# Performance work log

Hardware: AMD Instinct MI355X
Metric: run time of the kernel (lower is better)

Reference implementation:

```python
import jax, jax.numpy as jnp
import numpy as np

KS = 3          # image feature patch kernel size
RATE = 2        # downsample rate; alpha patches use kernel RATE*2, stride RATE
PENALTY = -10000.0
EPS = 1e-4
BN_EPS = 1e-5


def _pad(x, k, s):
    # reflect 'same' padding as in GCAModule.pad
    l = (k - s + 1) // 2
    r = (k - s) // 2
    return jnp.pad(x, ((0, 0), (0, 0), (l, r), (l, r)), mode='reflect')


def _extract_patches(x, k, s):
    # replicates reflect-pad + F.unfold + reshape -> (n, L, c, k, k)
    x = _pad(x, k, s)
    n, c, H, W = x.shape
    oh = (H - k) // s + 1
    ow = (W - k) // s + 1
    cols = [x[:, :, di:di + s * (oh - 1) + 1:s, dj:dj + s * (ow - 1) + 1:s]
            for di in range(k) for dj in range(k)]
    p = jnp.stack(cols, axis=2).reshape(n, c, k, k, oh * ow)  # (n,c,k,k,L)
    return jnp.transpose(p, (0, 4, 1, 2, 3))                  # (n,L,c,k,k)


def _deconv(score, kern):
    # torch: F.conv_transpose2d(score[None], kern, stride=RATE, padding=1) / 4
    # score: (L,h,w); kern: (L, ac, 4, 4) in torch conv_transpose (I,O,kh,kw) layout
    k = jnp.transpose(jnp.flip(kern, axis=(2, 3)), (1, 0, 2, 3))  # -> OIHW
    out = jax.lax.conv_general_dilated(
        score[None], k, window_strides=(1, 1), padding=[(2, 2), (2, 2)],
        lhs_dilation=(RATE, RATE), dimension_numbers=('NCHW', 'OIHW', 'NCHW'))
    return out[0] / 4.0


def gca_forward(img_feat, alpha_feat, unknown, gconv_w, gconv_b, oconv_w,
                bn_gamma, bn_beta):
    n = img_feat.shape[0]
    # guidance 1x1 conv + nearest downsample by RATE
    g = jnp.einsum('nchw,oc->nohw', img_feat, gconv_w) + gconv_b[None, :, None, None]
    g = g[:, :, ::RATE, ::RATE]
    u = unknown[:, :, ::RATE, ::RATE]
    # process_unknown_mask: per-sample softmax scales
    um = u.mean(axis=(2, 3))                                    # (n,1)
    km = 1.0 - um
    unknown_scale = jnp.clip(jnp.sqrt(um / km), 0.1, 10.0)      # (n,1)
    known_scale = jnp.clip(jnp.sqrt(km / um), 0.1, 10.0)        # (n,1)
    h, w = g.shape[2], g.shape[3]
    L = h * w
    img_ps = _extract_patches(g, KS, 1)                         # (n,L,c,3,3)
    alpha_ps = _extract_patches(alpha_feat, RATE * 2, RATE)     # (n,L,ac,4,4)
    unk_ps = _extract_patches(u, KS, 1)[:, :, 0].mean(axis=(2, 3))  # (n,L)
    # l2-normalized image patch kernels
    norm = jnp.sqrt(jnp.sum(img_ps * img_ps, axis=(2, 3, 4), keepdims=True))
    img_ps_n = img_ps / jnp.maximum(norm, EPS)
    # similarity: conv of padded g with patch kernels == patches-at-p . kernel-q
    sim = jnp.einsum('npckl,nqckl->nqp', img_ps, img_ps_n)      # (n,L,L)
    is_unknown = (unk_ps > 0.0).astype(sim.dtype)               # (n,L)
    scale = unknown_scale * is_unknown + known_scale * (1.0 - is_unknown)
    out = sim * scale[:, :, None]
    idx = jnp.arange(L)
    out = out.at[:, idx, idx].add(PENALTY * unk_ps)             # self-corr penalty
    gca = jax.nn.softmax(out, axis=1).reshape(n, L, h, w)
    prop = jax.vmap(_deconv)(gca, alpha_ps)                     # (n,ac,2h,2w)
    # out_conv: 1x1 conv (no bias) + BatchNorm (training stats) + residual
    y = jnp.einsum('nchw,oc->nohw', prop, oconv_w)
    mu = y.mean(axis=(0, 2, 3), keepdims=True)
    var = y.var(axis=(0, 2, 3), keepdims=True)
    y = (y - mu) / jnp.sqrt(var + BN_EPS)
    y = y * bn_gamma[None, :, None, None] + bn_beta[None, :, None, None]
    return y + alpha_feat


def setup_inputs():
    key = jax.random.key(0)
    ks = jax.random.split(key, 8)
    N, C, AC, H, W = 4, 256, 128, 64, 64
    img_feat = jax.random.normal(ks[0], (N, C, H, W), jnp.float32)
    alpha_feat = jax.random.normal(ks[1], (N, AC, H, W), jnp.float32)
    unknown = jax.random.randint(ks[2], (N, 1, H, W), 0, 2).astype(jnp.float32)
    gconv_w = jax.random.normal(ks[3], (C // 2, C), jnp.float32) / np.float32(np.sqrt(C))
    gconv_b = jax.random.normal(ks[4], (C // 2,), jnp.float32) * 0.01
    oconv_w = jax.random.normal(ks[5], (AC, AC), jnp.float32) / np.float32(np.sqrt(AC))
    bn_gamma = 0.001 + jax.random.normal(ks[6], (AC,), jnp.float32) * 0.001
    bn_beta = jax.random.normal(ks[7], (AC,), jnp.float32) * 0.001
    return dict(img_feat=img_feat, alpha_feat=alpha_feat, unknown=unknown,
                gconv_w=gconv_w, gconv_b=gconv_b, oconv_w=oconv_w,
                bn_gamma=bn_gamma, bn_beta=bn_beta)


def reference(img_feat, alpha_feat, unknown, gconv_w, gconv_b, oconv_w,
              bn_gamma, bn_beta):
    return gca_forward(img_feat, alpha_feat, unknown, gconv_w, gconv_b,
                       oconv_w, bn_gamma, bn_beta)
```

## Files before the change

### kernel.cpp

```cpp
#include <hip/hip_runtime.h>

#define NN 4
#define CIN 256
#define CH 128
#define HH 64
#define hh 32
#define L 1024
#define NB 2048
#define PENALTY -10000.0f
#define EPS 1e-4f

typedef __bf16 bf16x8 __attribute__((ext_vector_type(8)));
typedef float f32x4 __attribute__((ext_vector_type(4)));
typedef __attribute__((address_space(3))) void lds_t;
typedef __attribute__((address_space(1))) const void gbl_t;

__device__ __forceinline__ int refl32(int t) { return t < 0 ? -t : (t > 31 ? 62 - t : t); }
__device__ __forceinline__ int refl64(int t) { return t < 0 ? -t : (t > 63 ? 126 - t : t); }
__device__ __forceinline__ int swz(int k, int row) { return k ^ (((row >> 1) & 3) << 3); }

__global__ void k_prep(const float* __restrict__ img, const float* __restrict__ gw,
                       const float* __restrict__ ow, const float* __restrict__ unknown,
                       const float* __restrict__ alpha,
                       __bf16* __restrict__ Xb, __bf16* __restrict__ gwb,
                       __bf16* __restrict__ owb, float* __restrict__ unk,
                       float* __restrict__ scales, __bf16* __restrict__ Bt,
                       float* __restrict__ stats) {
    __shared__ float sm[CIN * 33];
    int bid = blockIdx.x, t = threadIdx.x;
    if (bid < 512) {
        int n = bid >> 7, o = bid & 127;
        const float* ap = alpha + ((size_t)(n * CH + o) << 12);
#pragma unroll
        for (int j = 0; j < 4; ++j) {
            int fi = t + j * 256;
            int row = fi >> 4, c4 = fi & 15;
            float4 v = *(const float4*)(ap + fi * 4);
            float* d = sm + row * 65 + c4 * 4;
            d[0] = v.x; d[1] = v.y; d[2] = v.z; d[3] = v.w;
        }
        __syncthreads();
        __bf16* Bn = Bt + ((size_t)(n * NB) << 10);
#pragma unroll
        for (int gi = 0; gi < 8; ++gi) {
            int g = gi * 256 + t;
            int ab = g >> 7, qg = g & 127;
            int a = ab >> 2, bb = ab & 3;
            int q0 = qg * 8;
            int qi = q0 >> 5, qj0 = q0 & 31;
            int ti = refl64(2 * qi + a - 1);
            const float* r = sm + ti * 65;
            __bf16 v[8];
#pragma unroll
            for (int s = 0; s < 8; ++s) v[s] = (__bf16)r[refl64(2 * (qj0 + s) + bb - 1)];
            int j = ab * 128 + o;
            *(bf16x8*)(Bn + ((size_t)j << 10) + swz(q0, j)) = *(bf16x8*)v;
        }
    } else if (bid < 640) {
        int idx = bid - 512;
        int i = idx & 31, n = idx >> 5;
        for (int e = t; e < CIN * 32; e += 256) {
            int c = e >> 5, jj = e & 31;
            sm[c * 33 + jj] = img[(((size_t)n * CIN + c) * HH + 2 * i) * HH + 2 * jj];
        }
        __syncthreads();
#pragma unroll
        for (int j = 0; j < 32; ++j) {
            int np = (n << 10) + i * 32 + j;
            int cl = swz(t, np);
            Xb[(size_t)np * CIN + t] = (__bf16)sm[cl * 33 + j];
        }
    } else if (bid < 644) {
        int n = bid - 640;
        float* u = sm;
        float* red = sm + 1024;
        float part = 0.f;
#pragma unroll
        for (int c = 0; c < 4; ++c) {
            int idx = t + c * 256;
            int i = idx >> 5, j = idx & 31;
            float v = unknown[n * 4096 + (2 * i) * HH + 2 * j];
            u[idx] = v;
            part += v;
        }
        red[t] = part;
        __syncthreads();
        for (int s = 128; s > 0; s >>= 1) {
            if (t < s) red[t] += red[t + s];
            __syncthreads();
        }
        if (t == 0) {
            float um = red[0] / 1024.0f;
            float km = 1.0f - um;
            scales[n * 2] = fminf(fmaxf(sqrtf(um / km), 0.1f), 10.0f);
            scales[n * 2 + 1] = fminf(fmaxf(sqrtf(km / um), 0.1f), 10.0f);
        }
#pragma unroll
        for (int c = 0; c < 4; ++c) {
            int idx = t + c * 256;
            int i = idx >> 5, j = idx & 31;
            float sum = 0.f;
#pragma unroll
            for (int di = -1; di <= 1; ++di)
#pragma unroll
                for (int dj = -1; dj <= 1; ++dj)
                    sum += u[refl32(i + di) * 32 + refl32(j + dj)];
            unk[n * L + idx] = sum * (1.0f / 9.0f);
        }
    } else {
        if (bid == 644) stats[t] = 0.f;
        for (int e = (bid - 644) * 256 + t; e < 49152; e += 36 * 256) {
            if (e < 32768) {
                int o = e >> 8, m = e & 255;
                gwb[e] = (__bf16)gw[o * 256 + swz(m, o)];
            } else {
                int e2 = e - 32768;
                int j = e2 >> 7, m = e2 & 127;
                owb[e2] = (__bf16)ow[j * 128 + swz(m, j)];
            }
        }
    }
}

__global__ __launch_bounds__(256, 2) void k_gemm0(const __bf16* __restrict__ Xb,
                                                  const __bf16* __restrict__ gwb,
                                                  const float* __restrict__ gb,
                                                  __bf16* __restrict__ gbf) {
    __shared__ __align__(16) __bf16 As[128 * 32];
    __shared__ __align__(16) __bf16 Bs[128 * 32];
    int p0 = blockIdx.x * 128;
    int t = threadIdx.x, l = t & 63, w = t >> 6;
    int wr = w >> 1, wc = w & 1;
    f32x4 acc[4][4] = {};
    for (int k0 = 0; k0 < CIN; k0 += 32) {
#pragma unroll
        for (int i = 0; i < 2; ++i) {
            const __bf16* srcA = Xb + (size_t)(p0 + i * 64 + (t >> 2)) * CIN + k0 + (t & 3) * 8;
            __builtin_amdgcn_global_load_lds((gbl_t*)srcA, (lds_t*)(As + i * 2048 + t * 8), 16, 0, 0);
            const __bf16* srcB = gwb + (size_t)(i * 64 + (t >> 2)) * CIN + k0 + (t & 3) * 8;
            __builtin_amdgcn_global_load_lds((gbl_t*)srcB, (lds_t*)(Bs + i * 2048 + t * 8), 16, 0, 0);
        }
        __syncthreads();
        int gl = l >> 4, r = l & 15;
        bf16x8 av[4], bv[4];
#pragma unroll
        for (int m = 0; m < 4; ++m) {
            int row = wr * 64 + m * 16 + r;
            av[m] = *(const bf16x8*)(As + row * 32 + swz(gl << 3, row));
            int col = wc * 64 + m * 16 + r;
            bv[m] = *(const bf16x8*)(Bs + col * 32 + swz(gl << 3, col));
        }
#pragma unroll
        for (int m = 0; m < 4; ++m)
#pragma unroll
            for (int c2 = 0; c2 < 4; ++c2)
                acc[m][c2] = __builtin_amdgcn_mfma_f32_16x16x32_bf16(av[m], bv[c2], acc[m][c2], 0, 0, 0);
        __syncthreads();
    }
    int r = l & 15, hi = l >> 4;
#pragma unroll
    for (int m = 0; m < 4; ++m)
#pragma unroll
        for (int c2 = 0; c2 < 4; ++c2) {
            int o = wc * 64 + c2 * 16 + r;
            float bias = gb[o];
#pragma unroll
            for (int reg = 0; reg < 4; ++reg) {
                int row = p0 + wr * 64 + m * 16 + hi * 4 + reg;
                gbf[((size_t)row << 7) + o] = (__bf16)(acc[m][c2][reg] + bias);
            }
        }
}

__global__ void k_ssqf(const __bf16* __restrict__ gbf, const float* __restrict__ unk,
                       const float* __restrict__ scales, float* __restrict__ f) {
    __shared__ float ssqs[1024];
    int n = blockIdx.x, t = threadIdx.x;
    {
        const __bf16* rp = gbf + (((size_t)(n << 10) + t) << 7);
        float s = 0.f;
#pragma unroll
        for (int kk = 0; kk < 16; ++kk) {
            bf16x8 v = *(const bf16x8*)(rp + kk * 8);
#pragma unroll
            for (int u2 = 0; u2 < 8; ++u2) {
                float x = (float)v[u2];
                s += x * x;
            }
        }
        ssqs[t] = s;
    }
    __syncthreads();
    float us = scales[n * 2], ks = scales[n * 2 + 1];
    int pi = t >> 5, pj = t & 31;
    float sum = 0.f;
#pragma unroll
    for (int di = -1; di <= 1; ++di)
#pragma unroll
        for (int dj = -1; dj <= 1; ++dj)
            sum += ssqs[refl32(pi + di) * 32 + refl32(pj + dj)];
    float norm = sqrtf(sum);
    float sc = unk[n * L + t] > 0.f ? us : ks;
    f[n * L + t] = sc / fmaxf(norm, EPS);
}

__global__ __launch_bounds__(256, 1) void k_gemm1(const __bf16* __restrict__ gbf,
                                                  const float* __restrict__ f,
                                                  const float* __restrict__ unk,
                                                  float* __restrict__ W) {
    __shared__ __align__(16) __bf16 As[4 * 6144];
    __shared__ __align__(16) __bf16 Bs[4 * 6144];
    int n = blockIdx.z;
    int p0 = blockIdx.y * 128, q0 = blockIdx.x * 128;
    const __bf16* gn = gbf + ((size_t)n << 17);
    int t = threadIdx.x, l = t & 63, w = t >> 6;
    int wr = w >> 1, wc = w & 1;
    int by4 = blockIdx.y * 4, bx4 = blockIdx.x * 4;
    int rbA = by4 - 1; rbA = rbA < 0 ? 0 : (rbA > 26 ? 26 : rbA);
    int rbB = bx4 - 1; rbB = rbB < 0 ? 0 : (rbB > 26 ? 26 : rbB);
#pragma unroll
    for (int k = 0; k < 12; ++k) {
        int chunk = k / 3;
        int rem = (k % 3) * 256 + t;
        int wrow = rem >> 2, sg = rem & 3;
        int so = (chunk << 5) + ((sg ^ ((wrow >> 1) & 3)) << 3);
        int grA = ((rbA + (wrow >> 5)) << 5) + (wrow & 31);
        __builtin_amdgcn_global_load_lds((gbl_t*)(gn + (size_t)grA * 128 + so),
                                         (lds_t*)(As + chunk * 6144 + rem * 8), 16, 0, 0);
        int grB = ((rbB + (wrow >> 5)) << 5) + (wrow & 31);
        __builtin_amdgcn_global_load_lds((gbl_t*)(gn + (size_t)grB * 128 + so),
                                         (lds_t*)(Bs + chunk * 6144 + rem * 8), 16, 0, 0);
    }
    __syncthreads();
    int gl = l >> 4, r = l & 15;
    int rpA[4][3], cpA[4][3], rpB[4][3], cpB[4][3];
#pragma unroll
    for (int m = 0; m < 4; ++m) {
        int prow = wr * 64 + m * 16 + r;
        int qrow = wc * 64 + m * 16 + r;
#pragma unroll
        for (int d = 0; d < 3; ++d) {
            rpA[m][d] = (refl32(by4 + (prow >> 5) + d - 1) - rbA) << 10;
            int cp = refl32((prow & 31) + d - 1);
            cpA[m][d] = cp * 32 + ((gl ^ ((cp >> 1) & 3)) << 3);
            rpB[m][d] = (refl32(bx4 + (qrow >> 5) + d - 1) - rbB) << 10;
            int cq = refl32((qrow & 31) + d - 1);
            cpB[m][d] = cq * 32 + ((gl ^ ((cq >> 1) & 3)) << 3);
        }
    }
    f32x4 acc[4][4] = {};
#pragma unroll
    for (int dk = 0; dk < 3; ++dk)
#pragma unroll
        for (int dl = 0; dl < 3; ++dl)
#pragma unroll
            for (int cc = 0; cc < 4; ++cc) {
                bf16x8 av[4], bv[4];
#pragma unroll
                for (int m = 0; m < 4; ++m) {
                    av[m] = *(const bf16x8*)(As + cc * 6144 + rpA[m][dk] + cpA[m][dl]);
                    bv[m] = *(const bf16x8*)(Bs + cc * 6144 + rpB[m][dk] + cpB[m][dl]);
                }
#pragma unroll
                for (int m = 0; m < 4; ++m)
#pragma unroll
                    for (int c2 = 0; c2 < 4; ++c2)
                        acc[m][c2] = __builtin_amdgcn_mfma_f32_16x16x32_bf16(av[m], bv[c2], acc[m][c2], 0, 0, 0);
            }
    int hi = l >> 4;
#pragma unroll
    for (int m = 0; m < 4; ++m)
#pragma unroll
        for (int c2 = 0; c2 < 4; ++c2) {
            int q = q0 + wc * 64 + c2 * 16 + r;
            float fq = f[n * L + q];
#pragma unroll
            for (int reg = 0; reg < 4; ++reg) {
                int p = p0 + wr * 64 + m * 16 + hi * 4 + reg;
                float val = acc[m][c2][reg] * fq;
                if (p == q) val += PENALTY * unk[n * L + p];
                W[((size_t)n << 20) + ((size_t)p << 10) + q] = val;
            }
        }
}

__global__ void k_softmax(const float* __restrict__ W, __bf16* __restrict__ Wb) {
    __shared__ float red[8];
    int row = blockIdx.x;
    int p = row & (L - 1);
    const float* Wr = W + (size_t)row * 1024;
    __bf16* Wbr = Wb + (size_t)row * 1024;
    int t = threadIdx.x, wv = t >> 6;
    float v[4];
    float mx = -1e30f;
#pragma unroll
    for (int ll = 0; ll < 4; ++ll) {
        v[ll] = Wr[t + ll * 256];
        mx = fmaxf(mx, v[ll]);
    }
#pragma unroll
    for (int off = 32; off > 0; off >>= 1) mx = fmaxf(mx, __shfl_xor(mx, off));
    if ((t & 63) == 0) red[wv] = mx;
    __syncthreads();
    mx = fmaxf(fmaxf(red[0], red[1]), fmaxf(red[2], red[3]));
    float sum = 0.f;
#pragma unroll
    for (int ll = 0; ll < 4; ++ll) {
        v[ll] = __expf(v[ll] - mx);
        sum += v[ll];
    }
#pragma unroll
    for (int off = 32; off > 0; off >>= 1) sum += __shfl_xor(sum, off);
    if ((t & 63) == 0) red[4 + wv] = sum;
    __syncthreads();
    float inv = 1.0f / (red[4] + red[5] + red[6] + red[7]);
#pragma unroll
    for (int ll = 0; ll < 4; ++ll) Wbr[swz(t + ll * 256, p)] = (__bf16)(v[ll] * inv);
}

__global__ __launch_bounds__(256, 2) void k_gemm2(const __bf16* __restrict__ Wb,
                                                  const __bf16* __restrict__ Bt,
                                                  __bf16* __restrict__ Tb) {
    int bid = blockIdx.x;
    int xcd = bid & 7, idx = bid >> 3;
    int n = xcd >> 1;
    int p0 = ((xcd & 1) * 4 + (idx & 3)) * 128;
    int j0 = (idx >> 2) * 128;
    __shared__ __align__(16) __bf16 As[4][4096];
    __shared__ __align__(16) __bf16 Bs[4][4096];
    const __bf16* An = Wb + ((size_t)n << 20);
    const __bf16* Bn = Bt + ((size_t)n * NB << 10);
    int t = threadIdx.x, l = t & 63, w = t >> 6;
    int wr = w >> 1, wc = w & 1;
    int gl = l >> 4, r = l & 15;
    f32x4 acc[4][4] = {};

    auto stage = [&](int buf, int k0) {
#pragma unroll
        for (int i = 0; i < 2; ++i) {
            int row = (t >> 2) + i * 64;
            int sgo = (t & 3) * 8;
            const __bf16* srcA = An + ((size_t)(p0 + row) << 10) + k0 + sgo;
            __builtin_amdgcn_global_load_lds((gbl_t*)srcA, (lds_t*)(&As[buf][row * 32 + sgo]), 16, 0, 0);
            const __bf16* srcB = Bn + ((size_t)(j0 + row) << 10) + k0 + sgo;
            __builtin_amdgcn_global_load_lds((gbl_t*)srcB, (lds_t*)(&Bs[buf][row * 32 + sgo]), 16, 0, 0);
        }
    };
    auto compute = [&](int buf) {
        bf16x8 av[4], bv[4];
#pragma unroll
        for (int m = 0; m < 4; ++m) {
            int row = wr * 64 + m * 16 + r;
            av[m] = *(const bf16x8*)(&As[buf][row * 32 + ((gl ^ ((row >> 1) & 3)) << 3)]);
            int col = wc * 64 + m * 16 + r;
            bv[m] = *(const bf16x8*)(&Bs[buf][col * 32 + ((gl ^ ((col >> 1) & 3)) << 3)]);
        }
#pragma unroll
        for (int m = 0; m < 4; ++m)
#pragma unroll
            for (int c2 = 0; c2 < 4; ++c2)
                acc[m][c2] = __builtin_amdgcn_mfma_f32_16x16x32_bf16(av[m], bv[c2], acc[m][c2], 0, 0, 0);
    };

    stage(0, 0);
    stage(1, 32);
    for (int it = 0; it < 32; ++it) {
        int buf = it & 3;
        if (it + 2 < 32) stage((it + 2) & 3, (it + 2) * 32);
        if (it < 30)
            asm volatile("s_waitcnt vmcnt(8)\n\ts_barrier" ::: "memory");
        else if (it == 30)
            asm volatile("s_waitcnt vmcnt(4)\n\ts_barrier" ::: "memory");
        else
            asm volatile("s_waitcnt vmcnt(0)\n\ts_barrier" ::: "memory");
        compute(buf);
    }
    int hi = l >> 4;
#pragma unroll
    for (int m = 0; m < 4; ++m)
#pragma unroll
        for (int c2 = 0; c2 < 4; ++c2) {
            int j = j0 + wc * 64 + c2 * 16 + r;
#pragma unroll
            for (int reg = 0; reg < 4; ++reg) {
                int p = p0 + wr * 64 + m * 16 + hi * 4 + reg;
                Tb[((size_t)n * L + p) * NB + j] = (__bf16)acc[m][c2][reg];
            }
        }
}

__global__ void k_oconv(const __bf16* __restrict__ owb, const __bf16* __restrict__ Tb,
                        float* __restrict__ y2, float* __restrict__ stats) {
    __shared__ __align__(16) __bf16 As[4 * 4096];
    __shared__ __align__(16) __bf16 Bp[4 * 2048];
    int n = blockIdx.z;
    int x0 = blockIdx.x * 64;
    int t = threadIdx.x, l = t & 63, w = t >> 6;
    int wr = w >> 1, wc = w & 1;
    int gl = l >> 4, r = l & 15, hi = l >> 4;
#pragma unroll
    for (int c = 0; c < 4; ++c)
#pragma unroll
        for (int i = 0; i < 2; ++i) {
            int h = i * 256 + t;
            const __bf16* src = owb + (size_t)(h >> 2) * CH + c * 32 + (h & 3) * 8;
            __builtin_amdgcn_global_load_lds((gbl_t*)src, (lds_t*)(As + c * 4096 + h * 8), 16, 0, 0);
        }
    const __bf16* Tn = Tb + ((size_t)(n * L) << 11);
#pragma unroll
    for (int it = 0; it < 4; ++it) {
        int e2 = it * 256 + t;
        int og = e2 & 15, pl = e2 >> 4;
        int pix = x0 + pl;
        int x = pix & 63, y = pix >> 6;
        float acc8[8] = {};
        int ap = (y + 1) & 1, bp = (x + 1) & 1;
#pragma unroll
        for (int da = 0; da < 2; ++da) {
            int a = ap + 2 * da;
            int ny = y + 1 - a;
            if (ny < 0 || ny >= 64) continue;
            int py = ny >> 1;
#pragma unroll
            for (int db = 0; db < 2; ++db) {
                int bb = bp + 2 * db;
                int nx = x + 1 - bb;
                if (nx < 0 || nx >= 64) continue;
                int px = nx >> 1;
                bf16x8 v = *(const bf16x8*)(Tn + (((size_t)(py * hh + px)) << 11) + (a * 4 + bb) * 128 + og * 8);
#pragma unroll
                for (int u2 = 0; u2 < 8; ++u2) acc8[u2] += (float)v[u2];
            }
        }
        __bf16 rr[8];
#pragma unroll
        for (int u2 = 0; u2 < 8; ++u2) rr[u2] = (__bf16)(acc8[u2] * 0.25f);
        int key = (pix >> 1) & 3;
        int dgl = (og & 3) ^ key;
        *(bf16x8*)(Bp + (og >> 2) * 2048 + pl * 32 + dgl * 8) = *(bf16x8*)rr;
    }
    __syncthreads();
    f32x4 acc[4][2] = {};
#pragma unroll
    for (int c = 0; c < 4; ++c) {
        bf16x8 av[4], bv[2];
#pragma unroll
        for (int m = 0; m < 4; ++m) {
            int row = wr * 64 + m * 16 + r;
            av[m] = *(const bf16x8*)(As + c * 4096 + row * 32 + ((gl ^ ((row >> 1) & 3)) << 3));
        }
#pragma unroll
        for (int c2 = 0; c2 < 2; ++c2) {
            int col = wc * 32 + c2 * 16 + r;
            bv[c2] = *(const bf16x8*)(Bp + c * 2048 + col * 32 + ((gl ^ ((col >> 1) & 3)) << 3));
        }
#pragma unroll
        for (int m = 0; m < 4; ++m)
#pragma unroll
            for (int c2 = 0; c2 < 2; ++c2)
                acc[m][c2] = __builtin_amdgcn_mfma_f32_16x16x32_bf16(av[m], bv[c2], acc[m][c2], 0, 0, 0);
    }
#pragma unroll
    for (int m = 0; m < 4; ++m)
#pragma unroll
        for (int c2 = 0; c2 < 2; ++c2) {
            int pix = x0 + wc * 32 + c2 * 16 + r;
#pragma unroll
            for (int reg = 0; reg < 4; ++reg) {
                int j = wr * 64 + m * 16 + hi * 4 + reg;
                y2[(((size_t)n * CH + j) << 12) + pix] = acc[m][c2][reg];
            }
        }
    __syncthreads();
    float* partS = (float*)As;
    float* partS2 = partS + 256;
#pragma unroll
    for (int m = 0; m < 4; ++m)
#pragma unroll
        for (int reg = 0; reg < 4; ++reg) {
            float s = 0.f, s2 = 0.f;
#pragma unroll
            for (int c2 = 0; c2 < 2; ++c2) {
                float v = acc[m][c2][reg];
                s += v;
                s2 += v * v;
            }
#pragma unroll
            for (int off = 1; off < 16; off <<= 1) {
                s += __shfl_xor(s, off);
                s2 += __shfl_xor(s2, off);
            }
            if (r == 0) {
                int j = wr * 64 + m * 16 + hi * 4 + reg;
                partS[j * 2 + wc] = s;
                partS2[j * 2 + wc] = s2;
            }
        }
    __syncthreads();
    if (t < 128) {
        atomicAdd(&stats[t * 2], partS[t * 2] + partS[t * 2 + 1]);
        atomicAdd(&stats[t * 2 + 1], partS2[t * 2] + partS2[t * 2 + 1]);
    }
}

__global__ void k_final(const float* __restrict__ y2, const float* __restrict__ stats,
                        const float* __restrict__ gamma, const float* __restrict__ beta,
                        const float* __restrict__ alpha, float* __restrict__ out) {
    int e4 = blockIdx.x * 256 + threadIdx.x;
    int oc = (e4 >> 10) & 127;
    float s1 = stats[oc * 2], s2 = stats[oc * 2 + 1];
    float mu = s1 * (1.0f / 16384.0f);
    float var = s2 * (1.0f / 16384.0f) - mu * mu;
    float inv = rsqrtf(var + 1e-5f);
    float g = gamma[oc], b = beta[oc];
    float4 yv = ((const float4*)y2)[e4];
    float4 av = ((const float4*)alpha)[e4];
    float4 o;
    o.x = (yv.x - mu) * inv * g + b + av.x;
    o.y = (yv.y - mu) * inv * g + b + av.y;
    o.z = (yv.z - mu) * inv * g + b + av.z;
    o.w = (yv.w - mu) * inv * g + b + av.w;
    ((float4*)out)[e4] = o;
}

extern "C" void kernel_launch(void* const* d_in, const int* in_sizes, int n_in,
                              void* d_out, int out_size, void* d_ws, size_t ws_size,
                              hipStream_t stream) {
    const float* img = (const float*)d_in[0];
    const float* alpha = (const float*)d_in[1];
    const float* unknown = (const float*)d_in[2];
    const float* gw = (const float*)d_in[3];
    const float* gb = (const float*)d_in[4];
    const float* ow = (const float*)d_in[5];
    const float* gamma = (const float*)d_in[6];
    const float* beta = (const float*)d_in[7];
    float* out = (float*)d_out;
    float* ws = (float*)d_ws;

    __bf16* Xb = (__bf16*)(ws);
    __bf16* gwb = (__bf16*)(ws + 524288);
    __bf16* owb = (__bf16*)(ws + 540672);
    __bf16* gbf = (__bf16*)(ws + 548864);
    float* f = ws + 811008;
    float* unk = ws + 815104;
    float* scales = ws + 819200;
    float* stats = ws + 819264;
    float* W = ws + 819520;
    __bf16* Wb = (__bf16*)(ws + 5013824);
    __bf16* Bt = (__bf16*)(ws + 7110976);
    __bf16* Tb = (__bf16*)(ws + 11305280);
    float* y2 = ws + 15499584;

    k_prep<<<680, 256, 0, stream>>>(img, gw, ow, unknown, alpha, Xb, gwb, owb, unk, scales, Bt, stats);
    k_gemm0<<<32, 256, 0, stream>>>(Xb, gwb, gb, gbf);
    k_ssqf<<<4, 1024, 0, stream>>>(gbf, unk, scales, f);
    k_gemm1<<<dim3(8, 8, 4), 256, 0, stream>>>(gbf, f, unk, W);
    k_softmax<<<4096, 256, 0, stream>>>(W, Wb);
    k_gemm2<<<512, 256, 0, stream>>>(Wb, Bt, Tb);
    k_oconv<<<dim3(64, 1, 4), 256, 0, stream>>>(owb, Tb, y2, stats);
    k_final<<<2048, 256, 0, stream>>>(y2, stats, gamma, beta, alpha, out);
}
```

Before: 102.7 us.

## Fuse patch-norm computation into gemm1, halve B staging, one row per wave softmax

Removes the separate k_ssqf launch: gemm1 now computes per-pixel sum of squares from its staged B tile and derives the per-column normalization scale in-block. The B operand is staged in two channel halves, which shrinks LDS so two blocks fit per CU (launch bounds raised to 2). The softmax kernel is rewritten to process one row per wavefront, with no shared-memory reductions or block barriers. The cost is extra barriers and a second staging phase in gemm1, plus redundant ssq work repeated across row tiles.

Result: faster. 92.65 us (-9.8%).

```diff
diff --git a/kernel.cpp b/kernel.cpp
--- a/kernel.cpp
+++ b/kernel.cpp
@@ -172,44 +172,15 @@
         }
 }
 
-__global__ void k_ssqf(const __bf16* __restrict__ gbf, const float* __restrict__ unk,
-                       const float* __restrict__ scales, float* __restrict__ f) {
-    __shared__ float ssqs[1024];
-    int n = blockIdx.x, t = threadIdx.x;
-    {
-        const __bf16* rp = gbf + (((size_t)(n << 10) + t) << 7);
-        float s = 0.f;
-#pragma unroll
-        for (int kk = 0; kk < 16; ++kk) {
-            bf16x8 v = *(const bf16x8*)(rp + kk * 8);
-#pragma unroll
-            for (int u2 = 0; u2 < 8; ++u2) {
-                float x = (float)v[u2];
-                s += x * x;
-            }
-        }
-        ssqs[t] = s;
-    }
-    __syncthreads();
-    float us = scales[n * 2], ks = scales[n * 2 + 1];
-    int pi = t >> 5, pj = t & 31;
-    float sum = 0.f;
-#pragma unroll
-    for (int di = -1; di <= 1; ++di)
-#pragma unroll
-        for (int dj = -1; dj <= 1; ++dj)
-            sum += ssqs[refl32(pi + di) * 32 + refl32(pj + dj)];
-    float norm = sqrtf(sum);
-    float sc = unk[n * L + t] > 0.f ? us : ks;
-    f[n * L + t] = sc / fmaxf(norm, EPS);
-}
-
-__global__ __launch_bounds__(256, 1) void k_gemm1(const __bf16* __restrict__ gbf,
-                                                  const float* __restrict__ f,
+__global__ __launch_bounds__(256, 2) void k_gemm1(const __bf16* __restrict__ gbf,
                                                   const float* __restrict__ unk,
+                                                  const float* __restrict__ scales,
                                                   float* __restrict__ W) {
-    __shared__ __align__(16) __bf16 As[4 * 6144];
-    __shared__ __align__(16) __bf16 Bs[4 * 6144];
+    __shared__ __align__(16) unsigned char RAW[75008];
+    __bf16* As1 = (__bf16*)RAW;
+    __bf16* Bh = (__bf16*)(RAW + 49152);
+    float* ssq = (float*)(RAW + 73728);
+    float* ftile = ssq + 192;
     int n = blockIdx.z;
     int p0 = blockIdx.y * 128, q0 = blockIdx.x * 128;
     const __bf16* gn = gbf + ((size_t)n << 17);
@@ -226,54 +197,103 @@
         int so = (chunk << 5) + ((sg ^ ((wrow >> 1) & 3)) << 3);
         int grA = ((rbA + (wrow >> 5)) << 5) + (wrow & 31);
         __builtin_amdgcn_global_load_lds((gbl_t*)(gn + (size_t)grA * 128 + so),
-                                         (lds_t*)(As + chunk * 6144 + rem * 8), 16, 0, 0);
-        int grB = ((rbB + (wrow >> 5)) << 5) + (wrow & 31);
-        __builtin_amdgcn_global_load_lds((gbl_t*)(gn + (size_t)grB * 128 + so),
-                                         (lds_t*)(Bs + chunk * 6144 + rem * 8), 16, 0, 0);
-    }
-    __syncthreads();
+                                         (lds_t*)(As1 + chunk * 6144 + rem * 8), 16, 0, 0);
+    }
+    auto stageB = [&](int h) {
+#pragma unroll
+        for (int k = 0; k < 6; ++k) {
+            int cl = k / 3;
+            int cc = 2 * h + cl;
+            int rem = (k % 3) * 256 + t;
+            int wrow = rem >> 2, sg = rem & 3;
+            int so = (cc << 5) + ((sg ^ ((wrow >> 1) & 3)) << 3);
+            int grB = ((rbB + (wrow >> 5)) << 5) + (wrow & 31);
+            __builtin_amdgcn_global_load_lds((gbl_t*)(gn + (size_t)grB * 128 + so),
+                                             (lds_t*)(Bh + cl * 6144 + rem * 8), 16, 0, 0);
+        }
+    };
+    stageB(0);
     int gl = l >> 4, r = l & 15;
-    int rpA[4][3], cpA[4][3], rpB[4][3], cpB[4][3];
+    int rpA_[4][3], cpA_[4][3], rpB_[4][3], cpB_[4][3];
 #pragma unroll
     for (int m = 0; m < 4; ++m) {
         int prow = wr * 64 + m * 16 + r;
         int qrow = wc * 64 + m * 16 + r;
 #pragma unroll
         for (int d = 0; d < 3; ++d) {
-            rpA[m][d] = (refl32(by4 + (prow >> 5) + d - 1) - rbA) << 10;
+            rpA_[m][d] = (refl32(by4 + (prow >> 5) + d - 1) - rbA) << 10;
             int cp = refl32((prow & 31) + d - 1);
-            cpA[m][d] = cp * 32 + ((gl ^ ((cp >> 1) & 3)) << 3);
-            rpB[m][d] = (refl32(bx4 + (qrow >> 5) + d - 1) - rbB) << 10;
+            cpA_[m][d] = cp * 32 + ((gl ^ ((cp >> 1) & 3)) << 3);
+            rpB_[m][d] = (refl32(bx4 + (qrow >> 5) + d - 1) - rbB) << 10;
             int cq = refl32((qrow & 31) + d - 1);
-            cpB[m][d] = cq * 32 + ((gl ^ ((cq >> 1) & 3)) << 3);
+            cpB_[m][d] = cq * 32 + ((gl ^ ((cq >> 1) & 3)) << 3);
         }
     }
     f32x4 acc[4][4] = {};
-#pragma unroll
-    for (int dk = 0; dk < 3; ++dk)
-#pragma unroll
-        for (int dl = 0; dl < 3; ++dl)
-#pragma unroll
-            for (int cc = 0; cc < 4; ++cc) {
-                bf16x8 av[4], bv[4];
-#pragma unroll
-                for (int m = 0; m < 4; ++m) {
-                    av[m] = *(const bf16x8*)(As + cc * 6144 + rpA[m][dk] + cpA[m][dl]);
-                    bv[m] = *(const bf16x8*)(Bs + cc * 6144 + rpB[m][dk] + cpB[m][dl]);
+    float ssqAcc = 0.f;
+    auto computeH = [&](int h) {
+#pragma unroll
+        for (int dk = 0; dk < 3; ++dk)
+#pragma unroll
+            for (int dl = 0; dl < 3; ++dl)
+#pragma unroll
+                for (int c = 0; c < 2; ++c) {
+                    int cc = 2 * h + c;
+                    bf16x8 av[4], bv[4];
+#pragma unroll
+                    for (int m = 0; m < 4; ++m) {
+                        av[m] = *(const bf16x8*)(As1 + cc * 6144 + rpA_[m][dk] + cpA_[m][dl]);
+                        bv[m] = *(const bf16x8*)(Bh + c * 6144 + rpB_[m][dk] + cpB_[m][dl]);
+                    }
+#pragma unroll
+                    for (int m = 0; m < 4; ++m)
+#pragma unroll
+                        for (int c2 = 0; c2 < 4; ++c2)
+                            acc[m][c2] = __builtin_amdgcn_mfma_f32_16x16x32_bf16(av[m], bv[c2], acc[m][c2], 0, 0, 0);
                 }
-#pragma unroll
-                for (int m = 0; m < 4; ++m)
-#pragma unroll
-                    for (int c2 = 0; c2 < 4; ++c2)
-                        acc[m][c2] = __builtin_amdgcn_mfma_f32_16x16x32_bf16(av[m], bv[c2], acc[m][c2], 0, 0, 0);
-            }
+        if (t < 192) {
+            int key = (t >> 1) & 3;
+#pragma unroll
+            for (int c = 0; c < 2; ++c)
+#pragma unroll
+                for (int g = 0; g < 4; ++g) {
+                    bf16x8 v = *(const bf16x8*)(Bh + c * 6144 + t * 32 + ((g ^ key) << 3));
+#pragma unroll
+                    for (int u2 = 0; u2 < 8; ++u2) {
+                        float x = (float)v[u2];
+                        ssqAcc += x * x;
+                    }
+                }
+        }
+    };
+    __syncthreads();
+    computeH(0);
+    __syncthreads();
+    stageB(1);
+    __syncthreads();
+    computeH(1);
+    if (t < 192) ssq[t] = ssqAcc;
+    __syncthreads();
+    if (t < 128) {
+        int q = q0 + t;
+        int qi = q >> 5, qj = q & 31;
+        float sum = 0.f;
+#pragma unroll
+        for (int di = -1; di <= 1; ++di)
+#pragma unroll
+            for (int dj = -1; dj <= 1; ++dj)
+                sum += ssq[(refl32(qi + di) - rbB) * 32 + refl32(qj + dj)];
+        float sc = unk[n * L + q] > 0.f ? scales[n * 2] : scales[n * 2 + 1];
+        ftile[t] = sc / fmaxf(sqrtf(sum), EPS);
+    }
+    __syncthreads();
     int hi = l >> 4;
 #pragma unroll
     for (int m = 0; m < 4; ++m)
 #pragma unroll
         for (int c2 = 0; c2 < 4; ++c2) {
             int q = q0 + wc * 64 + c2 * 16 + r;
-            float fq = f[n * L + q];
+            float fq = ftile[wc * 64 + c2 * 16 + r];
 #pragma unroll
             for (int reg = 0; reg < 4; ++reg) {
                 int p = p0 + wr * 64 + m * 16 + hi * 4 + reg;
@@ -285,37 +305,35 @@
 }
 
 __global__ void k_softmax(const float* __restrict__ W, __bf16* __restrict__ Wb) {
-    __shared__ float red[8];
-    int row = blockIdx.x;
+    int t = threadIdx.x, wv = t >> 6, lane = t & 63;
+    int row = blockIdx.x * 4 + wv;
+    const float* Wr = W + (size_t)row * 1024;
+    float v[16];
+    float mx = -1e30f;
+#pragma unroll
+    for (int k = 0; k < 16; ++k) {
+        v[k] = Wr[lane + k * 64];
+        mx = fmaxf(mx, v[k]);
+    }
+#pragma unroll
+    for (int off = 32; off > 0; off >>= 1) mx = fmaxf(mx, __shfl_xor(mx, off));
+    float sum = 0.f;
+#pragma unroll
+    for (int k = 0; k < 16; ++k) {
+        v[k] = __expf(v[k] - mx);
+        sum += v[k];
+    }
+#pragma unroll
+    for (int off = 32; off > 0; off >>= 1) sum += __shfl_xor(sum, off);
+    float inv = 1.0f / sum;
     int p = row & (L - 1);
-    const float* Wr = W + (size_t)row * 1024;
+    int key = ((p >> 1) & 3) << 3;
     __bf16* Wbr = Wb + (size_t)row * 1024;
-    int t = threadIdx.x, wv = t >> 6;
-    float v[4];
-    float mx = -1e30f;
-#pragma unroll
-    for (int ll = 0; ll < 4; ++ll) {
-        v[ll] = Wr[t + ll * 256];
-        mx = fmaxf(mx, v[ll]);
-    }
-#pragma unroll
-    for (int off = 32; off > 0; off >>= 1) mx = fmaxf(mx, __shfl_xor(mx, off));
-    if ((t & 63) == 0) red[wv] = mx;
-    __syncthreads();
-    mx = fmaxf(fmaxf(red[0], red[1]), fmaxf(red[2], red[3]));
-    float sum = 0.f;
-#pragma unroll
-    for (int ll = 0; ll < 4; ++ll) {
-        v[ll] = __expf(v[ll] - mx);
-        sum += v[ll];
-    }
-#pragma unroll
-    for (int off = 32; off > 0; off >>= 1) sum += __shfl_xor(sum, off);
-    if ((t & 63) == 0) red[4 + wv] = sum;
-    __syncthreads();
-    float inv = 1.0f / (red[4] + red[5] + red[6] + red[7]);
-#pragma unroll
-    for (int ll = 0; ll < 4; ++ll) Wbr[swz(t + ll * 256, p)] = (__bf16)(v[ll] * inv);
+#pragma unroll
+    for (int k = 0; k < 16; ++k) {
+        int idx = lane + k * 64;
+        Wbr[idx ^ key] = (__bf16)(v[k] * inv);
+    }
 }
 
 __global__ __launch_bounds__(256, 2) void k_gemm2(const __bf16* __restrict__ Wb,
@@ -541,7 +559,6 @@
     __bf16* gwb = (__bf16*)(ws + 524288);
     __bf16* owb = (__bf16*)(ws + 540672);
     __bf16* gbf = (__bf16*)(ws + 548864);
-    float* f = ws + 811008;
     float* unk = ws + 815104;
     float* scales = ws + 819200;
     float* stats = ws + 819264;
@@ -553,9 +570,8 @@
 
     k_prep<<<680, 256, 0, stream>>>(img, gw, ow, unknown, alpha, Xb, gwb, owb, unk, scales, Bt, stats);
     k_gemm0<<<32, 256, 0, stream>>>(Xb, gwb, gb, gbf);
-    k_ssqf<<<4, 1024, 0, stream>>>(gbf, unk, scales, f);
-    k_gemm1<<<dim3(8, 8, 4), 256, 0, stream>>>(gbf, f, unk, W);
-    k_softmax<<<4096, 256, 0, stream>>>(W, Wb);
+    k_gemm1<<<dim3(8, 8, 4), 256, 0, stream>>>(gbf, unk, scales, W);
+    k_softmax<<<1024, 256, 0, stream>>>(W, Wb);
     k_gemm2<<<512, 256, 0, stream>>>(Wb, Bt, Tb);
     k_oconv<<<dim3(64, 1, 4), 256, 0, stream>>>(owb, Tb, y2, stats);
     k_final<<<2048, 256, 0, stream>>>(y2, stats, gamma, beta, alpha, out);
```
